# Performance work log

Measured on AMD Instinct MI355X. Metric: run time of the kernel, lower is better.

## Reference

```python
import jax, jax.numpy as jnp
import numpy as np

DECAY = 0.99
EPS = 1e-06


def setup_inputs() -> dict:
    key = jax.random.key(0)
    k0, k1, k2, k3 = jax.random.split(key, 4)
    B, D, h, w = 1024, 64, 8, 8
    K, L = 512, h * w
    inp = jax.random.normal(k0, (B, D, h, w), dtype=jnp.float32)
    embedding = 0.01 * jax.random.normal(k1, (D, K, L), dtype=jnp.float32)
    dw = 0.01 * jax.random.normal(k2, (D, K, L), dtype=jnp.float32)
    cluster_size = 10.0 * jax.random.uniform(k3, (K, L), dtype=jnp.float32)
    return {"input": inp, "embedding": embedding, "dw": dw, "cluster_size": cluster_size}


def reference(input, embedding, dw, cluster_size):
    B, D, h, w = input.shape
    L = h * w
    K = embedding.shape[1]
    x = input.reshape(B, D, L)  # [B, D, L]

    # nearest-code assignment: argmin_k ||e[:,k,l] - x[b,:,l]||
    # ||x||^2 is constant over k, so argmin of ||e||^2 - 2<x,e> is equivalent
    e2 = jnp.sum(embedding * embedding, axis=0)              # [K, L]
    xe = jnp.einsum('bdl,dkl->bkl', x, embedding)            # [B, K, L]
    d2 = e2[None, :, :] - 2.0 * xe                           # [B, K, L]
    encoding_indices = jnp.argmin(d2, axis=1)                # [B, L]
    encoding = jax.nn.one_hot(encoding_indices, K, axis=1, dtype=x.dtype)  # [B, K, L]

    # decode: gather per-latent codebook entries (independent codebooks)
    emb_lkd = jnp.transpose(embedding, (2, 1, 0))            # [L, K, D]
    q = emb_lkd[jnp.arange(L)[None, :], encoding_indices]    # [B, L, D]
    q = jnp.transpose(q, (0, 2, 1))                          # [B, D, L]

    # EMA bookkeeping (training branch, independent_codebook=True)
    n = jnp.sum(cluster_size, axis=-1, keepdims=True) + 1e-06          # [K, 1]
    cs = (cluster_size + EPS) / (n + K * EPS) * n                      # [K, L]
    cs = DECAY * cs + (1.0 - DECAY) * jnp.sum(encoding, axis=0)        # [K, L]
    dw_batch = jnp.einsum('bkl,bdl->dkl', encoding, x)                 # [D, K, L]
    avg_probs = jnp.mean(encoding, axis=0)                             # [K, L]
    perplexity = jnp.exp(-jnp.sum(avg_probs * jnp.log(avg_probs + 1e-10), axis=0)) / K  # [L]
    dw_buf = DECAY * dw + (1.0 - DECAY) * (dw_batch / cs[None, :, :])  # [D, K, L]
    emb_new = DECAY * embedding + (1.0 - DECAY) * dw_buf               # [D, K, L]

    commitment_loss = jnp.mean((q - x) ** 2)
    quantized = (x + (q - x)).reshape(B, D, h, w)  # straight-through (value == q)
    encoding_out = encoding.reshape(B, K, h, w)
    return quantized, encoding_out, commitment_loss, perplexity, emb_new, dw_buf, cs
```

## Files before the change

### kernel.cpp

```cpp
#include <hip/hip_runtime.h>


typedef float f32x4 __attribute__((ext_vector_type(4)));

__global__ __launch_bounds__(256) void ktransE(const float* __restrict__ emb,
                                               float* __restrict__ eT,
                                               float* __restrict__ e2T,
                                               float* __restrict__ countsT,
                                               double* __restrict__ lossAcc) {
  const int k = blockIdx.x;
  const int t = threadIdx.x;
  __shared__ float s[64][65];
#pragma unroll
  for (int i = 0; i < 16; ++i) {
    int e = t + i * 256;
    int d = e >> 6, l = e & 63;
    s[d][l] = emb[d * 32768 + k * 64 + l];
  }
  __syncthreads();
  if (t < 64) {
    float s2 = 0.f;
#pragma unroll
    for (int d = 0; d < 64; ++d) {
      float v = s[d][t];
      s2 = __fadd_rn(s2, __fmul_rn(v, v));
    }
    e2T[t * 512 + k] = s2;
    countsT[k * 64 + t] = 0.f;
  }
  if (k == 0 && t == 0) lossAcc[0] = 0.0;
#pragma unroll
  for (int i = 0; i < 4; ++i) {
    int j = t + i * 256;
    int l = j >> 4, d0 = (j & 15) * 4;
    float4 w;
    w.x = s[d0][l]; w.y = s[d0 + 1][l]; w.z = s[d0 + 2][l]; w.w = s[d0 + 3][l];
    *(float4*)&eT[(l * 512 + k) * 64 + d0] = w;
  }
}

__global__ __launch_bounds__(256, 2) void kargmin(const float* __restrict__ x,
                                                  const float* __restrict__ eT,
                                                  const float* __restrict__ e2T,
                                                  int* __restrict__ idxout,
                                                  int* __restrict__ idxTout,
                                                  float* __restrict__ countsT) {
  const int l = blockIdx.y;
  const int b0 = blockIdx.x * 128;
  const int t = threadIdx.x;
  __shared__ float xs[128][68];
  __shared__ float es[128][68];
  __shared__ float e2s[128];
#pragma unroll
  for (int i = 0; i < 32; ++i) {
    int e = t + i * 256;
    int bl = e >> 6, d = e & 63;
    xs[bl][d] = x[(b0 + bl) * 4096 + d * 64 + l];
  }
  const int bg = t & 15;
  const int kg = t >> 4;
  float bestv[8];
  int bestk[8];
#pragma unroll
  for (int i = 0; i < 8; ++i) { bestv[i] = 3.4e38f; bestk[i] = 0; }

  for (int chunk = 0; chunk < 4; ++chunk) {
    __syncthreads();
    const float* src = eT + (l * 512 + chunk * 128) * 64;
#pragma unroll
    for (int i = 0; i < 8; ++i) {
      int f4 = t + i * 256;
      int r = f4 >> 4;
      int c = (f4 & 15) * 4;
      *(float4*)&es[r][c] = *(const float4*)&src[f4 * 4];
    }
    if (t < 128) e2s[t] = e2T[l * 512 + chunk * 128 + t];
    __syncthreads();

    float acc[8][8];
#pragma unroll
    for (int i = 0; i < 8; ++i)
#pragma unroll
      for (int j = 0; j < 8; ++j) acc[i][j] = 0.f;

    for (int d4 = 0; d4 < 16; ++d4) {
      float4 xv[8], ev[8];
#pragma unroll
      for (int i = 0; i < 8; ++i) xv[i] = *(const float4*)&xs[bg + i * 16][d4 * 4];
#pragma unroll
      for (int j = 0; j < 8; ++j) ev[j] = *(const float4*)&es[kg + j * 16][d4 * 4];
#pragma unroll
      for (int i = 0; i < 8; ++i)
#pragma unroll
        for (int j = 0; j < 8; ++j) {
          acc[i][j] = fmaf(xv[i].x, ev[j].x, acc[i][j]);
          acc[i][j] = fmaf(xv[i].y, ev[j].y, acc[i][j]);
          acc[i][j] = fmaf(xv[i].z, ev[j].z, acc[i][j]);
          acc[i][j] = fmaf(xv[i].w, ev[j].w, acc[i][j]);
        }
    }
#pragma unroll
    for (int j = 0; j < 8; ++j) {
      int kk = kg + j * 16;
      int kglob = chunk * 128 + kk;
      float e2v = e2s[kk];
#pragma unroll
      for (int i = 0; i < 8; ++i) {
        float d2 = fmaf(-2.0f, acc[i][j], e2v);
        if (d2 < bestv[i] || (d2 == bestv[i] && kglob < bestk[i])) {
          bestv[i] = d2; bestk[i] = kglob;
        }
      }
    }
  }
  __syncthreads();
  float* rv = &es[0][0];
  float* rkf = &xs[0][0];
#pragma unroll
  for (int i = 0; i < 8; ++i) {
    int bl = bg + i * 16;
    rv[bl * 16 + kg] = bestv[i];
    rkf[bl * 16 + kg] = (float)bestk[i];
  }
  __syncthreads();
  if (t < 128) {
    float bv = rv[t * 16];
    int bk = (int)rkf[t * 16];
#pragma unroll
    for (int g = 1; g < 16; ++g) {
      float v = rv[t * 16 + g];
      int kk = (int)rkf[t * 16 + g];
      if (v < bv || (v == bv && kk < bk)) { bv = v; bk = kk; }
    }
    idxout[(b0 + t) * 64 + l] = bk;
    idxTout[l * 1024 + b0 + t] = bk;
    unsafeAtomicAdd(&countsT[l * 512 + bk], 1.0f);
  }
}

__global__ __launch_bounds__(256) void kdwgather(const float* __restrict__ x,
                                                 const float* __restrict__ eT,
                                                 const int* __restrict__ idxb,
                                                 const int* __restrict__ idxT,
                                                 float* __restrict__ dwT,
                                                 float* __restrict__ out_q,
                                                 float* __restrict__ out_enc,
                                                 double* __restrict__ lossAcc) {
  const int t = threadIdx.x;
  __shared__ float SM[8192];
  if (blockIdx.x < 256) {
    const int l = blockIdx.x & 63;
    const int kq = (blockIdx.x >> 6) * 128;
    float* acc = SM;
#pragma unroll
    for (int i = 0; i < 32; ++i) acc[t + i * 256] = 0.f;
    const int w = t >> 6, lane = t & 63;
    __syncthreads();
    const int* idxl = idxT + l * 1024;
    for (int c = 0; c < 4; ++c) {
      const int base = w * 256 + c * 64;
      const int myidx = idxl[base + lane];
#pragma unroll 4
      for (int j = 0; j < 64; ++j) {
        int k = __shfl(myidx, j, 64) - kq;
        if ((unsigned)k < 128u) {
          float v = x[(base + j) * 4096 + lane * 64 + l];
          atomicAdd(&acc[(k << 6) + lane], v);
        }
      }
    }
    __syncthreads();
#pragma unroll
    for (int i = 0; i < 32; ++i) {
      int e = t + i * 256;
      int k = e >> 6, d = e & 63;
      dwT[((size_t)(kq + k) * 64 + l) * 64 + d] = acc[e];
    }
  } else {
    const int b = blockIdx.x - 256;
    float (*qb)[68] = (float (*)[68])SM;
    int* lidx = (int*)(SM + 4352);
    double* wsumS = (double*)(SM + 4432);
    if (t < 64) lidx[t] = idxb[b * 64 + t];
    __syncthreads();
    const int l = t >> 2, qd = (t & 3) * 16;
    const int kse = lidx[l];
    const float* ep = eT + (l * 512 + kse) * 64 + qd;
#pragma unroll
    for (int j = 0; j < 4; ++j) {
      float4 v = *(const float4*)&ep[j * 4];
      qb[qd + j * 4 + 0][l] = v.x;
      qb[qd + j * 4 + 1][l] = v.y;
      qb[qd + j * 4 + 2][l] = v.z;
      qb[qd + j * 4 + 3][l] = v.w;
    }
    __syncthreads();
    float ls = 0.f;
    const float* xp = x + b * 4096;
    float* op = out_q + b * 4096;
#pragma unroll
    for (int i = 0; i < 4; ++i) {
      int f4 = t + i * 256;
      float4 xv = *(const float4*)&xp[f4 * 4];
      int d = f4 >> 4, l0 = (f4 & 15) * 4;
      float4 qv = *(const float4*)&qb[d][l0];
      float4 dv, ov;
      dv.x = qv.x - xv.x; dv.y = qv.y - xv.y; dv.z = qv.z - xv.z; dv.w = qv.w - xv.w;
      ov.x = xv.x + dv.x; ov.y = xv.y + dv.y; ov.z = xv.z + dv.z; ov.w = xv.w + dv.w;
      *(float4*)&op[f4 * 4] = ov;
      ls = fmaf(dv.x, dv.x, ls); ls = fmaf(dv.y, dv.y, ls);
      ls = fmaf(dv.z, dv.z, ls); ls = fmaf(dv.w, dv.w, ls);
    }
    float* encp = out_enc + (size_t)b * 32768;
#pragma unroll
    for (int i = 0; i < 32; ++i) {
      int f4 = t + i * 256;
      int e = f4 * 4;
      int k = e >> 6, l0 = e & 63;
      f32x4 v;
      v.x = (lidx[l0 + 0] == k) ? 1.f : 0.f;
      v.y = (lidx[l0 + 1] == k) ? 1.f : 0.f;
      v.z = (lidx[l0 + 2] == k) ? 1.f : 0.f;
      v.w = (lidx[l0 + 3] == k) ? 1.f : 0.f;
      __builtin_nontemporal_store(v, (f32x4*)&encp[e]);
    }
#pragma unroll
    for (int off = 32; off > 0; off >>= 1) ls += __shfl_down(ls, off, 64);
    if ((t & 63) == 0) wsumS[t >> 6] = (double)ls;
    __syncthreads();
    if (t == 0) unsafeAtomicAdd(lossAcc, wsumS[0] + wsumS[1] + wsumS[2] + wsumS[3]);
  }
}

__global__ __launch_bounds__(256) void kemafinal(const float* __restrict__ cluster,
                                                 const float* __restrict__ countsT,
                                                 const float* __restrict__ dw,
                                                 const float* __restrict__ emb,
                                                 const float* __restrict__ dwT,
                                                 const double* __restrict__ lossAcc,
                                                 float* __restrict__ out_cs,
                                                 float* __restrict__ out_emb,
                                                 float* __restrict__ out_dwb,
                                                 float* __restrict__ out_loss,
                                                 float* __restrict__ out_perp) {
  const int t = threadIdx.x;
  if (blockIdx.x >= 512) {
    const int l = blockIdx.x - 512;
    if (t < 64) {
      float s = 0.f;
#pragma unroll
      for (int i = 0; i < 8; ++i) {
        int k = t * 8 + i;
        float p = countsT[l * 512 + k] * (1.0f / 1024.0f);
        s = __fadd_rn(s, __fmul_rn(p, logf(__fadd_rn(p, 1e-10f))));
      }
#pragma unroll
      for (int off = 32; off > 0; off >>= 1) s += __shfl_down(s, off, 64);
      if (t == 0) out_perp[l] = expf(-s) * (1.0f / 512.0f);
    }
    if (blockIdx.x == 512 && t == 64)
      out_loss[0] = (float)(lossAcc[0] / 4194304.0);
    return;
  }
  const int k = blockIdx.x;
  __shared__ float dwS[64][65];
  __shared__ float csS[64];
  __shared__ float nS;
  const float* sp = dwT + (size_t)k * 4096;
#pragma unroll
  for (int i = 0; i < 4; ++i) {
    int f4 = t + i * 256;
    float4 v = *(const float4*)&sp[f4 * 4];
    int l = f4 >> 4, d0 = (f4 & 15) * 4;
    dwS[l][d0] = v.x; dwS[l][d0 + 1] = v.y; dwS[l][d0 + 2] = v.z; dwS[l][d0 + 3] = v.w;
  }
  const float* cp = cluster + k * 64;
  if (t == 0) {
    float n = 0.f;
#pragma unroll
    for (int l = 0; l < 64; ++l) n = __fadd_rn(n, cp[l]);
    nS = __fadd_rn(n, 1e-06f);
  }
  __syncthreads();
  if (t < 64) {
    const float n = nS;
    const float denom = __fadd_rn(n, 0.000512f);
    float t1 = __fadd_rn(cp[t], 1e-06f);
    float r = __fdiv_rn(t1, denom);
    float r2 = __fmul_rn(r, n);
    float cs = __fadd_rn(__fmul_rn(0.99f, r2), __fmul_rn(0.01f, countsT[t * 512 + k]));
    csS[t] = cs;
    out_cs[k * 64 + t] = cs;
  }
  __syncthreads();
  const int l = t & 63;
  const int dlane = t >> 6;
#pragma unroll
  for (int r = 0; r < 16; ++r) {
    int d = r * 4 + dlane;
    int g = d * 32768 + k * 64 + l;
    float batch = dwS[l][d];
    float buf = 0.99f * dw[g] + 0.01f * (batch / csS[l]);
    out_dwb[g] = buf;
    out_emb[g] = 0.99f * emb[g] + 0.01f * buf;
  }
}

extern "C" void kernel_launch(void* const* d_in, const int* in_sizes, int n_in,
                              void* d_out, int out_size, void* d_ws, size_t ws_size,
                              hipStream_t stream) {
  (void)in_sizes; (void)n_in; (void)out_size; (void)ws_size;
  const float* x    = (const float*)d_in[0];
  const float* emb  = (const float*)d_in[1];
  const float* dw   = (const float*)d_in[2];
  const float* clus = (const float*)d_in[3];

  float* out = (float*)d_out;
  float* out_q    = out;
  float* out_enc  = out + 4194304;
  float* out_loss = out + 37748736;
  float* out_perp = out + 37748737;
  float* out_emb  = out + 37748801;
  float* out_dwb  = out + 39845953;
  float* out_cs   = out + 41943105;

  float* wsf = (float*)d_ws;
  float*  dwT     = wsf;
  float*  countsT = wsf + 2097152;
  float*  eT      = wsf + 2129920;
  float*  e2T     = wsf + 4227072;
  int*    idxb    = (int*)(wsf + 4259840);
  int*    idxT    = (int*)(wsf + 4325376);
  double* lossA   = (double*)(wsf + 4390912);

  ktransE<<<512, 256, 0, stream>>>(emb, eT, e2T, countsT, lossA);
  kargmin<<<dim3(8, 64), 256, 0, stream>>>(x, eT, e2T, idxb, idxT, countsT);
  kdwgather<<<1280, 256, 0, stream>>>(x, eT, idxb, idxT, dwT, out_q, out_enc, lossA);
  kemafinal<<<576, 256, 0, stream>>>(clus, countsT, dw, emb, dwT, lossA,
                                     out_cs, out_emb, out_dwb, out_loss, out_perp);
}
```

Measured before the change: 150.7 us.

## Stage transposed x in scratch and split dw scatter from gather kernel

kargmin now also writes a per-latent transposed copy of x, [L][B][D], into the out_enc buffer, which serves as scratch. A new kdw kernel uses 1024-thread blocks, each covering 256 codes, to accumulate dw from that layout with coalesced reads, replacing the strided reads of x in the old 256-block scatter. The q/encoding gather moves into its own kernel, which runs afterwards and overwrites the scratch. This adds a 16MB write plus an extra launch, and kdw has only 128 blocks of 64KB LDS each, so parallelism is lower.

Result: slower. 176.7 us (+17.3%).

```diff
diff --git a/kernel.cpp b/kernel.cpp
--- a/kernel.cpp
+++ b/kernel.cpp
@@ -44,18 +44,22 @@
                                                   const float* __restrict__ e2T,
                                                   int* __restrict__ idxout,
                                                   int* __restrict__ idxTout,
-                                                  float* __restrict__ countsT) {
+                                                  float* __restrict__ countsT,
+                                                  float* __restrict__ xT) {
   const int l = blockIdx.y;
   const int b0 = blockIdx.x * 128;
   const int t = threadIdx.x;
   __shared__ float xs[128][68];
   __shared__ float es[128][68];
   __shared__ float e2s[128];
+  float* xTl = xT + ((size_t)l * 1024 + b0) * 64;
 #pragma unroll
   for (int i = 0; i < 32; ++i) {
     int e = t + i * 256;
     int bl = e >> 6, d = e & 63;
-    xs[bl][d] = x[(b0 + bl) * 4096 + d * 64 + l];
+    float v = x[(b0 + bl) * 4096 + d * 64 + l];
+    xs[bl][d] = v;
+    xTl[e] = v;
   }
   const int bg = t & 15;
   const int kg = t >> 4;
@@ -138,98 +142,95 @@
   }
 }
 
-__global__ __launch_bounds__(256) void kdwgather(const float* __restrict__ x,
-                                                 const float* __restrict__ eT,
-                                                 const int* __restrict__ idxb,
-                                                 const int* __restrict__ idxT,
-                                                 float* __restrict__ dwT,
-                                                 float* __restrict__ out_q,
-                                                 float* __restrict__ out_enc,
-                                                 double* __restrict__ lossAcc) {
-  const int t = threadIdx.x;
-  __shared__ float SM[8192];
-  if (blockIdx.x < 256) {
-    const int l = blockIdx.x & 63;
-    const int kq = (blockIdx.x >> 6) * 128;
-    float* acc = SM;
-#pragma unroll
-    for (int i = 0; i < 32; ++i) acc[t + i * 256] = 0.f;
-    const int w = t >> 6, lane = t & 63;
-    __syncthreads();
-    const int* idxl = idxT + l * 1024;
-    for (int c = 0; c < 4; ++c) {
-      const int base = w * 256 + c * 64;
-      const int myidx = idxl[base + lane];
+__global__ __launch_bounds__(1024) void kdw(const float* __restrict__ xT,
+                                            const int* __restrict__ idxT,
+                                            float* __restrict__ dwT) {
+  const int l = blockIdx.y;
+  const int kh = blockIdx.x * 256;
+  const int t = threadIdx.x;
+  __shared__ float acc[256 * 64];
+#pragma unroll
+  for (int i = 0; i < 16; ++i) acc[t + i * 1024] = 0.f;
+  const int w = t >> 6, lane = t & 63;
+  const int sidxreg = idxT[l * 1024 + w * 64 + lane];
+  __syncthreads();
+  const float* xTl = xT + (size_t)l * 65536;
 #pragma unroll 4
-      for (int j = 0; j < 64; ++j) {
-        int k = __shfl(myidx, j, 64) - kq;
-        if ((unsigned)k < 128u) {
-          float v = x[(base + j) * 4096 + lane * 64 + l];
-          atomicAdd(&acc[(k << 6) + lane], v);
-        }
-      }
-    }
-    __syncthreads();
-#pragma unroll
-    for (int i = 0; i < 32; ++i) {
-      int e = t + i * 256;
-      int k = e >> 6, d = e & 63;
-      dwT[((size_t)(kq + k) * 64 + l) * 64 + d] = acc[e];
-    }
-  } else {
-    const int b = blockIdx.x - 256;
-    float (*qb)[68] = (float (*)[68])SM;
-    int* lidx = (int*)(SM + 4352);
-    double* wsumS = (double*)(SM + 4432);
-    if (t < 64) lidx[t] = idxb[b * 64 + t];
-    __syncthreads();
-    const int l = t >> 2, qd = (t & 3) * 16;
-    const int kse = lidx[l];
-    const float* ep = eT + (l * 512 + kse) * 64 + qd;
-#pragma unroll
-    for (int j = 0; j < 4; ++j) {
-      float4 v = *(const float4*)&ep[j * 4];
-      qb[qd + j * 4 + 0][l] = v.x;
-      qb[qd + j * 4 + 1][l] = v.y;
-      qb[qd + j * 4 + 2][l] = v.z;
-      qb[qd + j * 4 + 3][l] = v.w;
-    }
-    __syncthreads();
-    float ls = 0.f;
-    const float* xp = x + b * 4096;
-    float* op = out_q + b * 4096;
-#pragma unroll
-    for (int i = 0; i < 4; ++i) {
-      int f4 = t + i * 256;
-      float4 xv = *(const float4*)&xp[f4 * 4];
-      int d = f4 >> 4, l0 = (f4 & 15) * 4;
-      float4 qv = *(const float4*)&qb[d][l0];
-      float4 dv, ov;
-      dv.x = qv.x - xv.x; dv.y = qv.y - xv.y; dv.z = qv.z - xv.z; dv.w = qv.w - xv.w;
-      ov.x = xv.x + dv.x; ov.y = xv.y + dv.y; ov.z = xv.z + dv.z; ov.w = xv.w + dv.w;
-      *(float4*)&op[f4 * 4] = ov;
-      ls = fmaf(dv.x, dv.x, ls); ls = fmaf(dv.y, dv.y, ls);
-      ls = fmaf(dv.z, dv.z, ls); ls = fmaf(dv.w, dv.w, ls);
-    }
-    float* encp = out_enc + (size_t)b * 32768;
-#pragma unroll
-    for (int i = 0; i < 32; ++i) {
-      int f4 = t + i * 256;
-      int e = f4 * 4;
-      int k = e >> 6, l0 = e & 63;
-      f32x4 v;
-      v.x = (lidx[l0 + 0] == k) ? 1.f : 0.f;
-      v.y = (lidx[l0 + 1] == k) ? 1.f : 0.f;
-      v.z = (lidx[l0 + 2] == k) ? 1.f : 0.f;
-      v.w = (lidx[l0 + 3] == k) ? 1.f : 0.f;
-      __builtin_nontemporal_store(v, (f32x4*)&encp[e]);
-    }
-#pragma unroll
-    for (int off = 32; off > 0; off >>= 1) ls += __shfl_down(ls, off, 64);
-    if ((t & 63) == 0) wsumS[t >> 6] = (double)ls;
-    __syncthreads();
-    if (t == 0) unsafeAtomicAdd(lossAcc, wsumS[0] + wsumS[1] + wsumS[2] + wsumS[3]);
-  }
+  for (int j = 0; j < 64; ++j) {
+    int k = __shfl(sidxreg, j, 64) - kh;
+    if ((unsigned)k < 256u) {
+      float v = xTl[(w * 64 + j) * 64 + lane];
+      atomicAdd(&acc[(k << 6) + lane], v);
+    }
+  }
+  __syncthreads();
+#pragma unroll
+  for (int i = 0; i < 16; ++i) {
+    int e = t + i * 1024;
+    int k = e >> 6, d = e & 63;
+    dwT[((size_t)(kh + k) * 64 + l) * 64 + d] = acc[e];
+  }
+}
+
+__global__ __launch_bounds__(256) void kgather(const float* __restrict__ x,
+                                               const float* __restrict__ eT,
+                                               const int* __restrict__ idxin,
+                                               float* __restrict__ out_q,
+                                               float* __restrict__ out_enc,
+                                               double* __restrict__ lossAcc) {
+  const int b = blockIdx.x;
+  const int t = threadIdx.x;
+  __shared__ float qb[64][68];
+  __shared__ int lidx[64];
+  __shared__ double wsumS[4];
+  if (t < 64) lidx[t] = idxin[b * 64 + t];
+  __syncthreads();
+  const int l = t >> 2, qd = (t & 3) * 16;
+  const int kse = lidx[l];
+  const float* ep = eT + (l * 512 + kse) * 64 + qd;
+#pragma unroll
+  for (int j = 0; j < 4; ++j) {
+    float4 v = *(const float4*)&ep[j * 4];
+    qb[qd + j * 4 + 0][l] = v.x;
+    qb[qd + j * 4 + 1][l] = v.y;
+    qb[qd + j * 4 + 2][l] = v.z;
+    qb[qd + j * 4 + 3][l] = v.w;
+  }
+  __syncthreads();
+  float ls = 0.f;
+  const float* xp = x + b * 4096;
+  float* op = out_q + b * 4096;
+#pragma unroll
+  for (int i = 0; i < 4; ++i) {
+    int f4 = t + i * 256;
+    float4 xv = *(const float4*)&xp[f4 * 4];
+    int d = f4 >> 4, l0 = (f4 & 15) * 4;
+    float4 qv = *(const float4*)&qb[d][l0];
+    float4 dv, ov;
+    dv.x = qv.x - xv.x; dv.y = qv.y - xv.y; dv.z = qv.z - xv.z; dv.w = qv.w - xv.w;
+    ov.x = xv.x + dv.x; ov.y = xv.y + dv.y; ov.z = xv.z + dv.z; ov.w = xv.w + dv.w;
+    *(float4*)&op[f4 * 4] = ov;
+    ls = fmaf(dv.x, dv.x, ls); ls = fmaf(dv.y, dv.y, ls);
+    ls = fmaf(dv.z, dv.z, ls); ls = fmaf(dv.w, dv.w, ls);
+  }
+  float* encp = out_enc + (size_t)b * 32768;
+#pragma unroll
+  for (int i = 0; i < 32; ++i) {
+    int f4 = t + i * 256;
+    int e = f4 * 4;
+    int k = e >> 6, l0 = e & 63;
+    f32x4 v;
+    v.x = (lidx[l0 + 0] == k) ? 1.f : 0.f;
+    v.y = (lidx[l0 + 1] == k) ? 1.f : 0.f;
+    v.z = (lidx[l0 + 2] == k) ? 1.f : 0.f;
+    v.w = (lidx[l0 + 3] == k) ? 1.f : 0.f;
+    __builtin_nontemporal_store(v, (f32x4*)&encp[e]);
+  }
+#pragma unroll
+  for (int off = 32; off > 0; off >>= 1) ls += __shfl_down(ls, off, 64);
+  if ((t & 63) == 0) wsumS[t >> 6] = (double)ls;
+  __syncthreads();
+  if (t == 0) unsafeAtomicAdd(lossAcc, wsumS[0] + wsumS[1] + wsumS[2] + wsumS[3]);
 }
 
 __global__ __launch_bounds__(256) void kemafinal(const float* __restrict__ cluster,
@@ -333,9 +334,12 @@
   int*    idxT    = (int*)(wsf + 4325376);
   double* lossA   = (double*)(wsf + 4390912);
 
+  float* xT = out_enc;
+
   ktransE<<<512, 256, 0, stream>>>(emb, eT, e2T, countsT, lossA);
-  kargmin<<<dim3(8, 64), 256, 0, stream>>>(x, eT, e2T, idxb, idxT, countsT);
-  kdwgather<<<1280, 256, 0, stream>>>(x, eT, idxb, idxT, dwT, out_q, out_enc, lossA);
+  kargmin<<<dim3(8, 64), 256, 0, stream>>>(x, eT, e2T, idxb, idxT, countsT, xT);
+  kdw<<<dim3(2, 64), 1024, 0, stream>>>(xT, idxT, dwT);
+  kgather<<<1024, 256, 0, stream>>>(x, eT, idxb, out_q, out_enc, lossA);
   kemafinal<<<576, 256, 0, stream>>>(clus, countsT, dw, emb, dwT, lossA,
                                      out_cs, out_emb, out_dwb, out_loss, out_perp);
 }
```
